# Performance work log

Measured on AMD Instinct MI355X. Metric: run time of the kernel, lower is better.

## Reference

```python
import jax, jax.numpy as jnp
import numpy as np
from jax import lax

CAM_EDGE = 4096


def setup_inputs() -> dict:
    key = jax.random.key(0)
    x1 = jax.random.normal(key, (CAM_EDGE, CAM_EDGE), dtype=jnp.float32)
    return {"x1": x1}


def _label_components(mask):
    """4-connected component labeling via iterative min-label propagation.

    mask: [E, E] bool. Returns int32 [E, E] labels: each masked cell gets the
    minimum linear index of its connected component; unmasked cells get the
    sentinel N = E*E.
    """
    E = mask.shape[0]
    N = E * E
    sent = jnp.int32(N)
    init = jnp.where(mask, jnp.arange(N, dtype=jnp.int32).reshape(E, E), sent)
    sent_row = jnp.full((1, E), sent, dtype=jnp.int32)
    sent_col = jnp.full((E, 1), sent, dtype=jnp.int32)

    def propagate(lab):
        dn = jnp.concatenate([sent_row, lab[:-1]], axis=0)   # neighbor from above
        up = jnp.concatenate([lab[1:], sent_row], axis=0)    # neighbor from below
        lf = jnp.concatenate([sent_col, lab[:, :-1]], axis=1)
        rt = jnp.concatenate([lab[:, 1:], sent_col], axis=1)
        m = jnp.minimum(jnp.minimum(lab, up), jnp.minimum(dn, jnp.minimum(lf, rt)))
        return jnp.where(mask, m, sent)

    def cond(carry):
        _, changed = carry
        return changed

    def body(carry):
        lab, _ = carry
        new = propagate(lab)
        return new, jnp.any(new != lab)

    labels, _ = lax.while_loop(cond, body, (init, jnp.array(True)))
    return labels


def reference(x1):
    E = x1.shape[0]
    N = E * E
    v = jnp.tanh(x1)
    mask = v > 0
    labels = _label_components(mask)          # [E, E] int32, sentinel N for masked-out
    flat_lab = labels.reshape(-1)
    vflat = jnp.where(mask, v, 0.0).reshape(-1)
    ones = mask.reshape(-1).astype(v.dtype)
    # bucket N+1 collects the sentinel (non-positive cells); drop it
    sums = jax.ops.segment_sum(vflat, flat_lab, num_segments=N + 1)[:N]
    counts = jax.ops.segment_sum(ones, flat_lab, num_segments=N + 1)[:N]
    has = counts > 0                          # one True per connected component (its root index)
    per_comp = jnp.where(has, sums / (N + 1 - counts), 0.0)
    n_comp = jnp.sum(has.astype(v.dtype))
    total = jnp.sum(per_comp)
    return jnp.where(n_comp > 0, total / n_comp, 0.0)
```

## Files before the change

kernel.cpp:

```cpp
#include <hip/hip_runtime.h>

#define EDGE 4096
#define NPIX (EDGE * EDGE)
#define TILES_X 64
#define NTILES (TILES_X * TILES_X)
#define SLOTS 2048

typedef unsigned long long u64;

static __device__ __forceinline__ int g_load(int* L, int i) {
    return __hip_atomic_load(&L[i], __ATOMIC_RELAXED, __HIP_MEMORY_SCOPE_AGENT);
}
static __device__ __forceinline__ void g_store(int* L, int i, int v) {
    __hip_atomic_store(&L[i], v, __ATOMIC_RELAXED, __HIP_MEMORY_SCOPE_AGENT);
}
static __device__ int g_find(int* L, int i) {
    while (true) {
        const int p = g_load(L, i);
        if (p == i) return i;
        const int gp = g_load(L, p);
        if (gp == p) return p;
        g_store(L, i, gp);
        i = gp;
    }
}
static __device__ int g_unite(int* L, int a, int b) {
    while (true) {
        a = g_find(L, a); b = g_find(L, b);
        if (a == b) return 0;
        const int lo = a < b ? a : b;
        const int hi = a ^ b ^ lo;
        const int old = atomicMin(&L[hi], lo);
        if (old == hi) return 1;
        a = lo; b = old;
    }
}

static __device__ __forceinline__ int l_load(int* L, int i) {
    return __hip_atomic_load(&L[i], __ATOMIC_RELAXED, __HIP_MEMORY_SCOPE_WORKGROUP);
}
static __device__ __forceinline__ void l_store(int* L, int i, int v) {
    __hip_atomic_store(&L[i], v, __ATOMIC_RELAXED, __HIP_MEMORY_SCOPE_WORKGROUP);
}
static __device__ int l_find(int* L, int i) {
    while (true) {
        const int p = l_load(L, i);
        if (p == i) return i;
        const int gp = l_load(L, p);
        if (gp == p) return p;
        l_store(L, i, gp);
        i = gp;
    }
}
static __device__ void l_unite(int* L, int a, int b) {
    while (true) {
        a = l_find(L, a); b = l_find(L, b);
        if (a == b) return;
        const int lo = a < b ? a : b;
        const int hi = a ^ b ^ lo;
        const int old = atomicMin(&L[hi], lo);
        if (old == hi) return;
        a = lo; b = old;
    }
}

__global__ __launch_bounds__(256) void k_tile(const float* __restrict__ x,
                                              int* __restrict__ G,
                                              int* __restrict__ topM, int* __restrict__ botM,
                                              int* __restrict__ leftM, int* __restrict__ rightM,
                                              int* __restrict__ rootsArr,
                                              double* __restrict__ partials) {
    __shared__ u64 mrow[64];
    __shared__ u64 rstart[64];
    __shared__ unsigned int mpart[64][4];
    __shared__ int rowbase[64];
    __shared__ int P[SLOTS];
    __shared__ int wtot[4];
    __shared__ double wsum[4];
    __shared__ int Rtot;
    const int t = threadIdx.x;
    const int tile = blockIdx.x;
    const int tr = tile >> 6, tc = tile & 63;

    const int r = t >> 2, qd = t & 3;
    const float4* xp = reinterpret_cast<const float4*>(
        x + ((size_t)((tr << 6) | r) << 12) + (tc << 6) + (qd << 4));
    unsigned int m16 = 0;
    float sf = 0.0f;
    #pragma unroll
    for (int k = 0; k < 4; ++k) {
        const float4 a = xp[k];
        const float vv[4] = {a.x, a.y, a.z, a.w};
        #pragma unroll
        for (int j = 0; j < 4; ++j) {
            const float v = vv[j];
            if (v > 0.0f) {
                m16 |= 1u << (k * 4 + j);
                const float e = __expf(2.0f * v);
                sf += 1.0f - 2.0f * __builtin_amdgcn_rcpf(e + 1.0f);
            }
        }
    }
    mpart[r][qd] = m16;
    double s = (double)sf;
    for (int off = 32; off > 0; off >>= 1) s += __shfl_down(s, off, 64);
    if ((t & 63) == 0) wsum[t >> 6] = s;
    __syncthreads();

    if (t < 64) {
        const u64 m = (u64)mpart[t][0] | ((u64)mpart[t][1] << 16)
                    | ((u64)mpart[t][2] << 32) | ((u64)mpart[t][3] << 48);
        mrow[t] = m;
        const u64 rs = m & ~(m << 1);
        rstart[t] = rs;
        int inc = __popcll(rs);
        const int nr = inc;
        #pragma unroll
        for (int off = 1; off < 64; off <<= 1) {
            const int v = __shfl_up(inc, off, 64);
            if (t >= off) inc += v;
        }
        rowbase[t] = inc - nr;
        if (t == 63) Rtot = inc;
    }
    #pragma unroll
    for (int i = t; i < SLOTS; i += 256) P[i] = i;
    if (t == 0) partials[tile] = wsum[0] + wsum[1] + wsum[2] + wsum[3];
    __syncthreads();

    {
        const int rr = t >> 2;
        if (rr >= 1) {
            const u64 vm = mrow[rr] & mrow[rr - 1];
            u64 st = vm & ~(vm << 1);
            const int cb = (t & 3) * 16;
            st = (st >> cb) & 0xFFFFull;
            if (st) {
                const u64 rs  = rstart[rr];
                const u64 rsu = rstart[rr - 1];
                const int rb  = rowbase[rr];
                const int rbu = rowbase[rr - 1];
                do {
                    const int j = __builtin_ctzll(st) + cb;
                    const u64 thru = ~0ull >> (63 - j);
                    const int na = rb  + __popcll(rs  & thru) - 1;
                    const int nb = rbu + __popcll(rsu & thru) - 1;
                    const int old = atomicMin(&P[na], nb);
                    if (old != na && old != nb) l_unite(P, nb, old);
                    st &= st - 1;
                } while (st);
            }
        }
    }
    __syncthreads();

    const int R = Rtot;
    int broot = -1;
    {
        int rr, j;
        if (t < 64)       { rr = 0;       j = t; }
        else if (t < 128) { rr = 63;      j = t - 64; }
        else if (t < 192) { rr = t - 128; j = 0; }
        else              { rr = t - 192; j = 63; }
        if ((mrow[rr] >> j) & 1ull) {
            const int idx = __popcll(rstart[rr] & (~0ull >> (63 - j))) - 1;
            broot = l_find(P, rowbase[rr] + idx);
        }
    }
    int c = 0;
    for (int i = t; i < R; i += 256) c += (P[i] == i);
    int inc2 = c;
    #pragma unroll
    for (int off = 1; off < 64; off <<= 1) {
        const int v = __shfl_up(inc2, off, 64);
        if ((t & 63) >= off) inc2 += v;
    }
    if ((t & 63) == 63) wtot[t >> 6] = inc2;
    __syncthreads();

    const int w = t >> 6;
    int wbase = 0;
    if (w > 0) wbase += wtot[0];
    if (w > 1) wbase += wtot[1];
    if (w > 2) wbase += wtot[2];
    const int my_base = wbase + inc2 - c;
    const int nroots = wtot[0] + wtot[1] + wtot[2] + wtot[3];
    const int tileBase = tile * SLOTS;
    {
        int k = my_base;
        for (int i = t; i < R; i += 256) if (P[i] == i) P[i] = k++;
    }
    for (int i = t; i < nroots; i += 256) G[tileBase + i] = tileBase + i;
    __syncthreads();

    {
        const int node = (broot >= 0) ? (tileBase + P[broot]) : -1;
        const int bi = (tile << 6) | (t & 63);
        if (t < 64)       topM[bi]   = node;
        else if (t < 128) botM[bi]   = node;
        else if (t < 192) leftM[bi]  = node;
        else              rightM[bi] = node;
    }
    if (t == 0) rootsArr[tile] = nroots;
}

__global__ __launch_bounds__(128) void k_xmerge(const int* __restrict__ topM,
                                                const int* __restrict__ botM,
                                                const int* __restrict__ leftM,
                                                const int* __restrict__ rightM,
                                                int* G, int* __restrict__ linksArr) {
    __shared__ int lsum[2];
    const int t = threadIdx.x, tile = blockIdx.x;
    const int tr = tile >> 6, tc = tile & 63;
    int links = 0;
    if (t < 64) {
        if (tr > 0) {
            const int a = topM[(tile << 6) | t];
            const int b = botM[((tile - 64) << 6) | t];
            const int ap = __shfl_up(a, 1, 64);
            const int bp = __shfl_up(b, 1, 64);
            if ((a | b) >= 0) {
                const bool redund = (t > 0) && ((ap | bp) >= 0);
                if (!redund) links = g_unite(G, a, b);
            }
        }
    } else {
        const int rr = t - 64;
        if (tc > 0) {
            const int a = leftM[(tile << 6) | rr];
            const int b = rightM[((tile - 1) << 6) | rr];
            const int ap = __shfl_up(a, 1, 64);
            const int bp = __shfl_up(b, 1, 64);
            if ((a | b) >= 0) {
                const bool redund = (rr > 0) && ((ap | bp) >= 0);
                if (!redund) links = g_unite(G, a, b);
            }
        }
    }
    for (int off = 32; off > 0; off >>= 1) links += __shfl_down(links, off, 64);
    if ((t & 63) == 0) lsum[t >> 6] = links;
    __syncthreads();
    if (t == 0) linksArr[tile] = lsum[0] + lsum[1];
}

__global__ __launch_bounds__(256) void k_final(const double* __restrict__ partials,
                                               const int* __restrict__ rootsArr,
                                               const int* __restrict__ linksArr,
                                               float* __restrict__ out) {
    __shared__ double sd[256];
    __shared__ int si[256];
    const int t = threadIdx.x;
    double s = 0.0; int n = 0;
    for (int i = t; i < NTILES; i += 256) {
        s += partials[i];
        n += rootsArr[i] - linksArr[i];
    }
    sd[t] = s; si[t] = n; __syncthreads();
    for (int off = 128; off > 0; off >>= 1) {
        if (t < off) { sd[t] += sd[t + off]; si[t] += si[t + off]; }
        __syncthreads();
    }
    if (t == 0) {
        const int nn = si[0];
        out[0] = (nn > 0) ? (float)(sd[0] / (double)(NPIX + 1) / (double)nn) : 0.0f;
    }
}

extern "C" void kernel_launch(void* const* d_in, const int* in_sizes, int n_in,
                              void* d_out, int out_size, void* d_ws, size_t ws_size,
                              hipStream_t stream) {
    const float* x = (const float*)d_in[0];
    float* out = (float*)d_out;

    char* ws = (char*)d_ws;
    int* G = (int*)ws;
    int* topM   = (int*)(ws + (32u << 20));
    int* botM   = topM  + NTILES * 64;
    int* leftM  = botM  + NTILES * 64;
    int* rightM = leftM + NTILES * 64;
    double* partials = (double*)(ws + (36u << 20));
    int* rootsArr = (int*)(ws + (36u << 20) + (64u << 10));
    int* linksArr = (int*)(ws + (36u << 20) + (80u << 10));

    k_tile  <<<NTILES, 256, 0, stream>>>(x, G, topM, botM, leftM, rightM,
                                         rootsArr, partials);
    k_xmerge<<<NTILES, 128, 0, stream>>>(topM, botM, leftM, rightM, G, linksArr);
    k_final <<<1, 256, 0, stream>>>(partials, rootsArr, linksArr, out);
}
```

Baseline: 56.08 us.

## Split tanh/mask pass into streaming prep kernel writing packed bitmask

Moves the input read, tanh sum and mask building out of the per-tile labeling kernel into a separate grid-stride kernel. That kernel reads the input with contiguous coalesced loads and writes a packed 1-bit-per-pixel mask. The labeling kernel then loads one 64-bit word per tile row instead of 64 rows of float strips. This aims for better bandwidth on the dominant read and a lighter labeling kernel, at the cost of an extra launch and a small mask round-trip through memory. The tanh partial sums are now accumulated in float per block before being converted to double.

New measurement: 59.51 us. 1.06x slower.

```diff
diff --git a/kernel.cpp b/kernel.cpp
--- a/kernel.cpp
+++ b/kernel.cpp
@@ -2,9 +2,9 @@
 
 #define EDGE 4096
 #define NPIX (EDGE * EDGE)
-#define TILES_X 64
-#define NTILES (TILES_X * TILES_X)
+#define NTILES 4096
 #define SLOTS 2048
+#define PREP_BLOCKS 2048
 
 typedef unsigned long long u64;
 
@@ -64,52 +64,53 @@
     }
 }
 
-__global__ __launch_bounds__(256) void k_tile(const float* __restrict__ x,
-                                              int* __restrict__ G,
-                                              int* __restrict__ topM, int* __restrict__ botM,
-                                              int* __restrict__ leftM, int* __restrict__ rightM,
-                                              int* __restrict__ rootsArr,
+__global__ __launch_bounds__(256) void k_prep(const float* __restrict__ x,
+                                              unsigned char* __restrict__ maskb,
                                               double* __restrict__ partials) {
+    __shared__ float wsumf[4];
+    float sf = 0.0f;
+    const int stride = gridDim.x * blockDim.x;
+    for (int p = blockIdx.x * blockDim.x + threadIdx.x; p < NPIX / 8; p += stride) {
+        const float4 a0 = reinterpret_cast<const float4*>(x)[p * 2];
+        const float4 a1 = reinterpret_cast<const float4*>(x)[p * 2 + 1];
+        const float v[8] = {a0.x, a0.y, a0.z, a0.w, a1.x, a1.y, a1.z, a1.w};
+        unsigned int m = 0;
+        #pragma unroll
+        for (int j = 0; j < 8; ++j) {
+            const float vj = v[j];
+            if (vj > 0.0f) {
+                m |= 1u << j;
+                const float e = __expf(2.0f * vj);
+                sf += 1.0f - 2.0f * __builtin_amdgcn_rcpf(e + 1.0f);
+            }
+        }
+        maskb[p] = (unsigned char)m;
+    }
+    for (int off = 32; off > 0; off >>= 1) sf += __shfl_down(sf, off, 64);
+    if ((threadIdx.x & 63) == 0) wsumf[threadIdx.x >> 6] = sf;
+    __syncthreads();
+    if (threadIdx.x == 0)
+        partials[blockIdx.x] =
+            (double)wsumf[0] + (double)wsumf[1] + (double)wsumf[2] + (double)wsumf[3];
+}
+
+__global__ __launch_bounds__(256) void k_ccl(const u64* __restrict__ M,
+                                             int* __restrict__ G,
+                                             int* __restrict__ topM, int* __restrict__ botM,
+                                             int* __restrict__ leftM, int* __restrict__ rightM,
+                                             int* __restrict__ rootsArr) {
     __shared__ u64 mrow[64];
     __shared__ u64 rstart[64];
-    __shared__ unsigned int mpart[64][4];
     __shared__ int rowbase[64];
     __shared__ int P[SLOTS];
     __shared__ int wtot[4];
-    __shared__ double wsum[4];
     __shared__ int Rtot;
     const int t = threadIdx.x;
     const int tile = blockIdx.x;
     const int tr = tile >> 6, tc = tile & 63;
 
-    const int r = t >> 2, qd = t & 3;
-    const float4* xp = reinterpret_cast<const float4*>(
-        x + ((size_t)((tr << 6) | r) << 12) + (tc << 6) + (qd << 4));
-    unsigned int m16 = 0;
-    float sf = 0.0f;
-    #pragma unroll
-    for (int k = 0; k < 4; ++k) {
-        const float4 a = xp[k];
-        const float vv[4] = {a.x, a.y, a.z, a.w};
-        #pragma unroll
-        for (int j = 0; j < 4; ++j) {
-            const float v = vv[j];
-            if (v > 0.0f) {
-                m16 |= 1u << (k * 4 + j);
-                const float e = __expf(2.0f * v);
-                sf += 1.0f - 2.0f * __builtin_amdgcn_rcpf(e + 1.0f);
-            }
-        }
-    }
-    mpart[r][qd] = m16;
-    double s = (double)sf;
-    for (int off = 32; off > 0; off >>= 1) s += __shfl_down(s, off, 64);
-    if ((t & 63) == 0) wsum[t >> 6] = s;
-    __syncthreads();
-
     if (t < 64) {
-        const u64 m = (u64)mpart[t][0] | ((u64)mpart[t][1] << 16)
-                    | ((u64)mpart[t][2] << 32) | ((u64)mpart[t][3] << 48);
+        const u64 m = M[(((tr << 6) | t) << 6) | tc];
         mrow[t] = m;
         const u64 rs = m & ~(m << 1);
         rstart[t] = rs;
@@ -125,7 +126,6 @@
     }
     #pragma unroll
     for (int i = t; i < SLOTS; i += 256) P[i] = i;
-    if (t == 0) partials[tile] = wsum[0] + wsum[1] + wsum[2] + wsum[3];
     __syncthreads();
 
     {
@@ -251,10 +251,8 @@
     __shared__ int si[256];
     const int t = threadIdx.x;
     double s = 0.0; int n = 0;
-    for (int i = t; i < NTILES; i += 256) {
-        s += partials[i];
-        n += rootsArr[i] - linksArr[i];
-    }
+    for (int i = t; i < PREP_BLOCKS; i += 256) s += partials[i];
+    for (int i = t; i < NTILES; i += 256) n += rootsArr[i] - linksArr[i];
     sd[t] = s; si[t] = n; __syncthreads();
     for (int off = 128; off > 0; off >>= 1) {
         if (t < off) { sd[t] += sd[t + off]; si[t] += si[t + off]; }
@@ -278,12 +276,14 @@
     int* botM   = topM  + NTILES * 64;
     int* leftM  = botM  + NTILES * 64;
     int* rightM = leftM + NTILES * 64;
-    double* partials = (double*)(ws + (36u << 20));
-    int* rootsArr = (int*)(ws + (36u << 20) + (64u << 10));
-    int* linksArr = (int*)(ws + (36u << 20) + (80u << 10));
-
-    k_tile  <<<NTILES, 256, 0, stream>>>(x, G, topM, botM, leftM, rightM,
-                                         rootsArr, partials);
+    unsigned char* maskb = (unsigned char*)(ws + (36u << 20));
+    double* partials = (double*)(ws + (38u << 20));
+    int* rootsArr = (int*)(ws + (38u << 20) + (64u << 10));
+    int* linksArr = (int*)(ws + (38u << 20) + (80u << 10));
+
+    k_prep  <<<PREP_BLOCKS, 256, 0, stream>>>(x, maskb, partials);
+    k_ccl   <<<NTILES, 256, 0, stream>>>((const u64*)maskb, G,
+                                         topM, botM, leftM, rightM, rootsArr);
     k_xmerge<<<NTILES, 128, 0, stream>>>(topM, botM, leftM, rightM, G, linksArr);
     k_final <<<1, 256, 0, stream>>>(partials, rootsArr, linksArr, out);
 }
```
